# Performance work log

Hardware: AMD Instinct MI355X
Metric: run time of the kernel (lower is better)

Reference implementation:

```python
import jax, jax.numpy as jnp
import numpy as np

# GemNet sizes
N_EDGES = 80_000
N_TRIP = 640_000      # intermediate triplets (cbf rows)
N_QUAD = 1_280_000    # quadruplets
KMAX = 24             # max quadruplets per edge (padded)
NUM_SPH = 7
E_EDGE, E_QUAD, E_BIL, E_RBF, E_CBF, E_SBF = 128, 64, 64, 16, 16, 32

INV_SQRT_2 = 1.0 / np.sqrt(2.0)
SILU_SCALE = 1.0 / 0.6  # GemNet ScaledSiLU


def scaled_silu(x):
    return jax.nn.silu(x) * SILU_SCALE


def setup_inputs() -> dict:
    key = jax.random.key(0)
    ks = jax.random.split(key, 16)
    s = 0.05
    inp = {
        'm': jax.random.normal(ks[0], (N_EDGES, E_EDGE), jnp.float32),
        'rbf': jax.random.normal(ks[1], (N_EDGES, E_RBF), jnp.float32),
        'cbf': jax.random.normal(ks[2], (N_TRIP, E_CBF), jnp.float32),
        'sbf_W1': jax.random.normal(ks[3], (N_EDGES, E_SBF, NUM_SPH), jnp.float32) * s,
        'sbf_sph': jax.random.normal(ks[4], (N_EDGES, KMAX, NUM_SPH), jnp.float32) * s,
        # consistent ragged indexing: quadruplet q maps to edge q%N_EDGES at slot q//N_EDGES (< KMAX)
        'Kidx4': jnp.arange(N_QUAD, dtype=jnp.int32) // N_EDGES,
        'id4_reduce_ca': jnp.arange(N_QUAD, dtype=jnp.int32) % N_EDGES,
        'id_swap': jnp.arange(N_EDGES, dtype=jnp.int32).reshape(-1, 2)[:, ::-1].reshape(-1),
        'id4_expand_intm_db': jax.random.randint(ks[5], (N_TRIP,), 0, N_EDGES, jnp.int32),
        'id4_expand_abd': jax.random.randint(ks[6], (N_QUAD,), 0, N_TRIP, jnp.int32),
        # parameters (Dense layers are bias-free)
        'W_dense_db': jax.random.normal(ks[7], (E_EDGE, E_EDGE), jnp.float32) * s,
        'W_rbf': jax.random.normal(ks[8], (E_RBF, E_EDGE), jnp.float32) * s,
        'W_cbf': jax.random.normal(ks[9], (E_CBF, E_QUAD), jnp.float32) * s,
        'W_down': jax.random.normal(ks[10], (E_EDGE, E_QUAD), jnp.float32) * s,
        'W_bil': jax.random.normal(ks[11], (E_QUAD, E_SBF, E_BIL), jnp.float32) * s,
        'W_up_ca': jax.random.normal(ks[12], (E_BIL, E_EDGE), jnp.float32) * s,
        'W_up_ac': jax.random.normal(ks[13], (E_BIL, E_EDGE), jnp.float32) * s,
    }
    return inp


def reference(m, rbf, cbf, sbf_W1, sbf_sph,
              W_dense_db, W_rbf, W_cbf, W_down, W_bil, W_up_ca, W_up_ac,
              Kidx4, id_swap, id4_reduce_ca, id4_expand_intm_db, id4_expand_abd):
    # dense_db + Hadamard with projected rbf (ScalingFactor scale == 1.0 with scale_file=None)
    x_db = scaled_silu(m @ W_dense_db)           # (nEdges, E_EDGE)
    x_db = x_db * (rbf @ W_rbf)                  # scale_rbf (scale=1)
    x_db = scaled_silu(x_db @ W_down)            # (nEdges, E_QUAD)
    x_db = x_db[id4_expand_intm_db]              # (nTrip, E_QUAD)
    x_db = x_db * (cbf @ W_cbf)                  # scale_cbf (scale=1)
    x_db = x_db[id4_expand_abd]                  # (nQuad, E_QUAD)

    # EfficientInteractionBilinear: scatter quadruplets into (nEdges, Kmax, E_QUAD)
    n_edges, kmax = sbf_sph.shape[0], sbf_sph.shape[1]
    m2 = jnp.zeros((n_edges, kmax, x_db.shape[1]), x_db.dtype)
    m2 = m2.at[id4_reduce_ca, Kidx4].set(x_db)
    sum_k = jnp.einsum('eks,ekc->esc', sbf_sph, m2)    # (nEdges, NUM_SPH, E_QUAD)
    t = jnp.einsum('eis,esc->eic', sbf_W1, sum_k)      # (nEdges, E_SBF, E_QUAD)
    x = jnp.einsum('eic,cio->eo', t, W_bil)            # (nEdges, E_BIL); scale_sbf_sum (scale=1)

    x_ca = scaled_silu(x @ W_up_ca)              # (nEdges, E_EDGE)
    x_ac = scaled_silu(x @ W_up_ac)[id_swap]
    return (x_ca + x_ac) * INV_SQRT_2
```

## Files before the change

kernel.cpp:

```cpp
#include <hip/hip_runtime.h>
#include <hip/hip_bf16.h>

#define NEDGES 80000
#define NTRIP  640000
#define NQUAD  1280000

typedef __attribute__((ext_vector_type(8))) short short8;
typedef __attribute__((ext_vector_type(4))) float f32x4;
typedef __attribute__((ext_vector_type(2))) _Float16 half2v;
typedef __attribute__((ext_vector_type(8))) _Float16 half8v;

__device__ __forceinline__ unsigned short f2bf(float f) {
  __hip_bfloat16 h = __float2bfloat16(f);
  return reinterpret_cast<unsigned short&>(h);
}
__device__ __forceinline__ float bf2f(short s) {
  union { unsigned u; float f; } u;
  u.u = ((unsigned)(unsigned short)s) << 16;
  return u.f;
}
__device__ __forceinline__ float sSiLU(float x) {
  return x * (1.0f / 0.6f) / (1.0f + __expf(-x));
}

__device__ __forceinline__ void pack_one(const float* __restrict__ W,
                                         unsigned short* __restrict__ dst,
                                         int p, int NT, int Ksrc, int N) {
  int j = p & 7;
  int l = (p >> 3) & 63;
  int rest = p >> 9;
  int nt = rest % NT;
  int kb = rest / NT;
  int k = kb * 32 + ((l >> 4) << 3) + j;
  int n = nt * 16 + (l & 15);
  float v = (k < Ksrc) ? W[(size_t)k * N + n] : 0.0f;
  dst[p] = f2bf(v);
}

__global__ __launch_bounds__(256) void kpack(
    const float* __restrict__ Wd, const float* __restrict__ Wrbf,
    const float* __restrict__ Wdown, const float* __restrict__ Wbil,
    const float* __restrict__ Wupca, const float* __restrict__ Wupac,
    unsigned short* __restrict__ WdP, unsigned short* __restrict__ WrbfP,
    unsigned short* __restrict__ WdownP, unsigned short* __restrict__ WbilP,
    unsigned short* __restrict__ WupcaP, unsigned short* __restrict__ WupacP) {
  int idx = blockIdx.x * 256 + threadIdx.x;
  if (idx < 16384)        pack_one(Wd,    WdP,    idx,          8, 128,  128);
  else if (idx < 20480)   pack_one(Wrbf,  WrbfP,  idx - 16384,  8, 16,   128);
  else if (idx < 28672)   pack_one(Wdown, WdownP, idx - 20480,  4, 128,  64);
  else if (idx < 159744)  pack_one(Wbil,  WbilP,  idx - 28672,  4, 2048, 64);
  else if (idx < 167936)  pack_one(Wupca, WupcaP, idx - 159744, 8, 64,   128);
  else if (idx < 176128)  pack_one(Wupac, WupacP, idx - 167936, 8, 64,   128);
}

__global__ __launch_bounds__(256) void kA(
    const float* __restrict__ m, const float* __restrict__ rbf,
    const unsigned short* __restrict__ WdP, const unsigned short* __restrict__ WrbfP,
    const unsigned short* __restrict__ WdownP, unsigned short* __restrict__ x_down) {
  __shared__ unsigned short h_lds[4][16][136];
  const int tid = threadIdx.x;
  const int w = tid >> 6, l = tid & 63;
  const int el = l & 15, g = l >> 4;
  const int ebase = blockIdx.x * 64 + w * 16;

  short8 am[4];
  {
    const float* mrow = m + (size_t)(ebase + el) * 128 + g * 8;
#pragma unroll
    for (int kb = 0; kb < 4; ++kb) {
      const f32x4 lo = *reinterpret_cast<const f32x4*>(mrow + kb * 32);
      const f32x4 hi = *reinterpret_cast<const f32x4*>(mrow + kb * 32 + 4);
      short8 a;
      a[0] = f2bf(lo[0]); a[1] = f2bf(lo[1]); a[2] = f2bf(lo[2]); a[3] = f2bf(lo[3]);
      a[4] = f2bf(hi[0]); a[5] = f2bf(hi[1]); a[6] = f2bf(hi[2]); a[7] = f2bf(hi[3]);
      am[kb] = a;
    }
  }
  short8 ar;
  {
    const float* rrow = rbf + (size_t)(ebase + el) * 16 + (g & 1) * 8;
    const f32x4 lo = *reinterpret_cast<const f32x4*>(rrow);
    const f32x4 hi = *reinterpret_cast<const f32x4*>(rrow + 4);
    ar[0] = f2bf(lo[0]); ar[1] = f2bf(lo[1]); ar[2] = f2bf(lo[2]); ar[3] = f2bf(lo[3]);
    ar[4] = f2bf(hi[0]); ar[5] = f2bf(hi[1]); ar[6] = f2bf(hi[2]); ar[7] = f2bf(hi[3]);
  }

  f32x4 acc1[8], acc2[8];
  const f32x4 z = {0.f, 0.f, 0.f, 0.f};
#pragma unroll
  for (int nt = 0; nt < 8; ++nt) { acc1[nt] = z; acc2[nt] = z; }

#pragma unroll
  for (int kb = 0; kb < 4; ++kb) {
#pragma unroll
    for (int nt = 0; nt < 8; ++nt) {
      short8 b = *reinterpret_cast<const short8*>(WdP + (((kb * 8 + nt) * 64 + l) << 3));
      acc1[nt] = __builtin_amdgcn_mfma_f32_16x16x32_bf16(am[kb], b, acc1[nt], 0, 0, 0);
    }
  }
#pragma unroll
  for (int nt = 0; nt < 8; ++nt) {
    short8 b = *reinterpret_cast<const short8*>(WrbfP + ((nt * 64 + l) << 3));
    acc2[nt] = __builtin_amdgcn_mfma_f32_16x16x32_bf16(ar, b, acc2[nt], 0, 0, 0);
  }

#pragma unroll
  for (int nt = 0; nt < 8; ++nt)
#pragma unroll
    for (int r = 0; r < 4; ++r) {
      float h = sSiLU(acc1[nt][r]) * acc2[nt][r];
      h_lds[w][g * 4 + r][nt * 16 + el] = f2bf(h);
    }
  __syncthreads();

  f32x4 acc3[4];
#pragma unroll
  for (int nt = 0; nt < 4; ++nt) acc3[nt] = z;
#pragma unroll
  for (int kb = 0; kb < 4; ++kb) {
    short8 a = *reinterpret_cast<const short8*>(&h_lds[w][el][kb * 32 + g * 8]);
#pragma unroll
    for (int nt = 0; nt < 4; ++nt) {
      short8 b = *reinterpret_cast<const short8*>(WdownP + (((kb * 4 + nt) * 64 + l) << 3));
      acc3[nt] = __builtin_amdgcn_mfma_f32_16x16x32_bf16(a, b, acc3[nt], 0, 0, 0);
    }
  }
#pragma unroll
  for (int nt = 0; nt < 4; ++nt)
#pragma unroll
    for (int r = 0; r < 4; ++r)
      x_down[(size_t)(ebase + g * 4 + r) * 64 + nt * 16 + el] = f2bf(sSiLU(acc3[nt][r]));
}

__global__ __launch_bounds__(256) void kG(
    const float* __restrict__ cbf, const int* __restrict__ intm,
    const unsigned short* __restrict__ x_down, const float* __restrict__ Wcbf,
    unsigned short* __restrict__ y) {
  __shared__ float cbf_lds[4][16][16];
  const int tid = threadIdx.x;
  const int w = tid >> 6, c = tid & 63;
  const int wid = blockIdx.x * 4 + w;

  float wc[16];
#pragma unroll
  for (int r = 0; r < 16; ++r) wc[r] = Wcbf[r * 64 + c];

#pragma unroll
  for (int it = 0; it < 4; ++it) {
    const int t0 = (wid * 4 + it) * 16;

    const int ivv = intm[t0 + (c & 15)];
    const f32x4 cq = *reinterpret_cast<const f32x4*>(
        cbf + (size_t)(t0 + (c >> 2)) * 16 + (c & 3) * 4);
    *reinterpret_cast<f32x4*>(&cbf_lds[w][c >> 2][(c & 3) * 4]) = cq;

    int es[16];
#pragma unroll
    for (int k = 0; k < 16; ++k) es[k] = __builtin_amdgcn_readlane(ivv, k);

    unsigned short xr[16];
#pragma unroll
    for (int k = 0; k < 16; ++k) xr[k] = x_down[(size_t)es[k] * 64 + c];

#pragma unroll
    for (int j = 0; j < 16; ++j) {
      const f32x4* cr = reinterpret_cast<const f32x4*>(&cbf_lds[w][j][0]);
      const f32x4 q0 = cr[0], q1 = cr[1], q2 = cr[2], q3 = cr[3];
      float proj = 0.f;
#pragma unroll
      for (int r = 0; r < 4; ++r) {
        proj = fmaf(q0[r], wc[r], proj);
        proj = fmaf(q1[r], wc[4 + r], proj);
        proj = fmaf(q2[r], wc[8 + r], proj);
        proj = fmaf(q3[r], wc[12 + r], proj);
      }
      y[(size_t)(t0 + j) * 64 + c] = f2bf(bf2f((short)xr[j]) * proj);
    }
  }
}

__global__ __launch_bounds__(256) void kS2(
    const float* __restrict__ sph, const int* __restrict__ abd,
    const unsigned short* __restrict__ y, unsigned short* __restrict__ sumk) {
  __shared__ float sph_lds[4][172];
  const int tid = threadIdx.x;
  const int w = tid >> 6, c = tid & 63;
  const int wid = blockIdx.x * 4 + w;

#pragma unroll
  for (int it = 0; it < 8; ++it) {
    const int e = wid * 8 + it;

    const int tvv = abd[(size_t)(c & 15) * NEDGES + e];
    if (c < 42)
      *reinterpret_cast<f32x4*>(&sph_lds[w][c * 4]) =
          *reinterpret_cast<const f32x4*>(sph + (size_t)e * 168 + c * 4);

    int te[16];
#pragma unroll
    for (int k = 0; k < 16; ++k) te[k] = __builtin_amdgcn_readlane(tvv, k);

    unsigned short yv[16];
#pragma unroll
    for (int k = 0; k < 16; ++k) yv[k] = y[(size_t)te[k] * 64 + c];

    float sk[7] = {0.f, 0.f, 0.f, 0.f, 0.f, 0.f, 0.f};
#pragma unroll
    for (int k = 0; k < 16; ++k) {
      const float row = bf2f((short)yv[k]);
#pragma unroll
      for (int s = 0; s < 7; ++s) sk[s] = fmaf(sph_lds[w][k * 7 + s], row, sk[s]);
    }
    half8v sv;
#pragma unroll
    for (int s = 0; s < 7; ++s) sv[s] = (_Float16)sk[s];
    sv[7] = (_Float16)0.f;
    *reinterpret_cast<half8v*>(sumk + (size_t)e * 512 + c * 8) = sv;
  }
}

__global__ __launch_bounds__(256) void kS(
    const float* __restrict__ cbf, const float* __restrict__ sph,
    const int* __restrict__ abd, const int* __restrict__ intm,
    const unsigned short* __restrict__ x_down, const float* __restrict__ Wcbf,
    unsigned short* __restrict__ sumk) {
  __shared__ float cbf_lds[4][16][16];
  __shared__ int   te_lds[4][16];
  __shared__ float sph_lds[4][172];
  const int tid = threadIdx.x;
  const int w = tid >> 6, c = tid & 63;
  const int e = blockIdx.x * 4 + w;

  const int tvv = abd[(size_t)(c & 15) * NEDGES + e];
  if (c < 42)
    *reinterpret_cast<f32x4*>(&sph_lds[w][c * 4]) =
        *reinterpret_cast<const f32x4*>(sph + (size_t)e * 168 + c * 4);
  const int ivv = intm[tvv];
  if (c < 16) te_lds[w][c] = tvv;

  float wc[16];
#pragma unroll
  for (int r = 0; r < 16; ++r) wc[r] = Wcbf[r * 64 + c];

  int es[16];
#pragma unroll
  for (int k = 0; k < 16; ++k) es[k] = __builtin_amdgcn_readlane(ivv, k);

  const int tq = te_lds[w][c >> 2];
  const f32x4 cq = *reinterpret_cast<const f32x4*>(cbf + (size_t)tq * 16 + (c & 3) * 4);

  unsigned short xr[16];
#pragma unroll
  for (int k = 0; k < 16; ++k) xr[k] = x_down[(size_t)es[k] * 64 + c];

  *reinterpret_cast<f32x4*>(&cbf_lds[w][c >> 2][(c & 3) * 4]) = cq;

  float sk[7] = {0.f, 0.f, 0.f, 0.f, 0.f, 0.f, 0.f};
#pragma unroll
  for (int k = 0; k < 16; ++k) {
    const f32x4* cr = reinterpret_cast<const f32x4*>(&cbf_lds[w][k][0]);
    const f32x4 q0 = cr[0], q1 = cr[1], q2 = cr[2], q3 = cr[3];
    float proj = 0.f;
#pragma unroll
    for (int r = 0; r < 4; ++r) {
      proj = fmaf(q0[r], wc[r], proj);
      proj = fmaf(q1[r], wc[4 + r], proj);
      proj = fmaf(q2[r], wc[8 + r], proj);
      proj = fmaf(q3[r], wc[12 + r], proj);
    }
    const float row = bf2f((short)xr[k]) * proj;
#pragma unroll
    for (int s = 0; s < 7; ++s) sk[s] = fmaf(sph_lds[w][k * 7 + s], row, sk[s]);
  }
  short8 sv;
#pragma unroll
  for (int s = 0; s < 7; ++s) sv[s] = (short)f2bf(sk[s]);
  sv[7] = 0;
  *reinterpret_cast<short8*>(sumk + (size_t)e * 512 + c * 8) = sv;
}

__global__ __launch_bounds__(256, 4) void kB3(
    const float* __restrict__ sbfW1, const unsigned short* __restrict__ sumk,
    const unsigned short* __restrict__ WbilP, float* __restrict__ xpart) {
  __shared__ unsigned short stg[4][2][16][72];
  const int tid = threadIdx.x;
  const int w = tid >> 6, l = tid & 63;
  const int el = l & 15, g = l >> 4;
  const int gw = blockIdx.x * 4 + w;
  const int eb = gw >> 1, kh = gw & 1;
  const int ebase = eb * 16;
  const int sr = l >> 3, sq = l & 7;

  half2v w1h[32];
  {
    float w1f[56];
    const f32x4* wp = reinterpret_cast<const f32x4*>(sbfW1 + (size_t)(ebase + el) * 224 + g * 56);
#pragma unroll
    for (int qq = 0; qq < 14; ++qq) {
      f32x4 v = wp[qq];
      w1f[qq * 4 + 0] = v[0]; w1f[qq * 4 + 1] = v[1];
      w1f[qq * 4 + 2] = v[2]; w1f[qq * 4 + 3] = v[3];
    }
#pragma unroll
    for (int j = 0; j < 8; ++j) {
#pragma unroll
      for (int p = 0; p < 3; ++p) {
        half2v h;
        h[0] = (_Float16)w1f[j * 7 + 2 * p];
        h[1] = (_Float16)w1f[j * 7 + 2 * p + 1];
        w1h[j * 4 + p] = h;
      }
      half2v h;
      h[0] = (_Float16)w1f[j * 7 + 6];
      h[1] = (_Float16)0.f;
      w1h[j * 4 + 3] = h;
    }
  }

  const unsigned short* base = sumk + (size_t)ebase * 512 + kh * 256;
  short8 ld0 = *reinterpret_cast<const short8*>(base + (size_t)sr * 512 + sq * 8);
  short8 ld1 = *reinterpret_cast<const short8*>(base + (size_t)(sr + 8) * 512 + sq * 8);

  short8 bn0, bn1, bn2, bn3;
  {
    const unsigned short* bp = WbilP + (((kh * 32 * 4) * 64 + l) << 3);
    bn0 = *reinterpret_cast<const short8*>(bp);
    bn1 = *reinterpret_cast<const short8*>(bp + (64 << 3));
    bn2 = *reinterpret_cast<const short8*>(bp + (128 << 3));
    bn3 = *reinterpret_cast<const short8*>(bp + (192 << 3));
  }

  const f32x4 z = {0.f, 0.f, 0.f, 0.f};
  f32x4 acc[4];
#pragma unroll
  for (int nt = 0; nt < 4; ++nt) acc[nt] = z;

#pragma unroll
  for (int s = 0; s < 4; ++s) {
    const int b = s & 1;
    *reinterpret_cast<short8*>(&stg[w][b][sr][sq * 8]) = ld0;
    *reinterpret_cast<short8*>(&stg[w][b][sr + 8][sq * 8]) = ld1;
    if (s < 3) {
      ld0 = *reinterpret_cast<const short8*>(base + (size_t)sr * 512 + (s + 1) * 64 + sq * 8);
      ld1 = *reinterpret_cast<const short8*>(base + (size_t)(sr + 8) * 512 + (s + 1) * 64 + sq * 8);
    }
#pragma unroll
    for (int kk = 0; kk < 8; ++kk) {
      const short8 bc0 = bn0, bc1 = bn1, bc2 = bn2, bc3 = bn3;
      if (!(s == 3 && kk == 7)) {
        const int kbn = kh * 32 + s * 8 + kk + 1;
        const unsigned short* bp = WbilP + (((kbn * 4) * 64 + l) << 3);
        bn0 = *reinterpret_cast<const short8*>(bp);
        bn1 = *reinterpret_cast<const short8*>(bp + (64 << 3));
        bn2 = *reinterpret_cast<const short8*>(bp + (128 << 3));
        bn3 = *reinterpret_cast<const short8*>(bp + (192 << 3));
      }

      const half8v skv = *reinterpret_cast<const half8v*>(&stg[w][b][el][kk * 8]);
      half2v sp0, sp1, sp2, sp3;
      sp0[0] = skv[0]; sp0[1] = skv[1];
      sp1[0] = skv[2]; sp1[1] = skv[3];
      sp2[0] = skv[4]; sp2[1] = skv[5];
      sp3[0] = skv[6]; sp3[1] = skv[7];

      short8 a;
#pragma unroll
      for (int j = 0; j < 8; ++j) {
        float t = 0.f;
        t = __builtin_amdgcn_fdot2(w1h[j * 4 + 0], sp0, t, false);
        t = __builtin_amdgcn_fdot2(w1h[j * 4 + 1], sp1, t, false);
        t = __builtin_amdgcn_fdot2(w1h[j * 4 + 2], sp2, t, false);
        t = __builtin_amdgcn_fdot2(w1h[j * 4 + 3], sp3, t, false);
        a[j] = (short)f2bf(t);
      }
      acc[0] = __builtin_amdgcn_mfma_f32_16x16x32_bf16(a, bc0, acc[0], 0, 0, 0);
      acc[1] = __builtin_amdgcn_mfma_f32_16x16x32_bf16(a, bc1, acc[1], 0, 0, 0);
      acc[2] = __builtin_amdgcn_mfma_f32_16x16x32_bf16(a, bc2, acc[2], 0, 0, 0);
      acc[3] = __builtin_amdgcn_mfma_f32_16x16x32_bf16(a, bc3, acc[3], 0, 0, 0);
    }
  }

  float* po = xpart + (size_t)kh * (NEDGES * 64);
#pragma unroll
  for (int nt = 0; nt < 4; ++nt)
#pragma unroll
    for (int r = 0; r < 4; ++r)
      po[(size_t)(ebase + g * 4 + r) * 64 + nt * 16 + el] = acc[nt][r];
}

__global__ __launch_bounds__(256) void kU(
    const float* __restrict__ xpart, const unsigned short* __restrict__ WupcaP,
    const unsigned short* __restrict__ WupacP, float* __restrict__ out) {
  const int tid = threadIdx.x;
  const int w = tid >> 6, l = tid & 63;
  const int el = l & 15, g = l >> 4;
  const int ebase = (blockIdx.x * 4 + w) * 16;

  const float* p0 = xpart + (size_t)(ebase + el) * 64;
  const float* p1 = p0 + (size_t)NEDGES * 64;

  const f32x4 z = {0.f, 0.f, 0.f, 0.f};
  f32x4 aca[8], acb[8];
#pragma unroll
  for (int nt = 0; nt < 8; ++nt) { aca[nt] = z; acb[nt] = z; }

#pragma unroll
  for (int kb = 0; kb < 2; ++kb) {
    const f32x4 a0 = *reinterpret_cast<const f32x4*>(p0 + kb * 32 + g * 8);
    const f32x4 a1 = *reinterpret_cast<const f32x4*>(p0 + kb * 32 + g * 8 + 4);
    const f32x4 b0 = *reinterpret_cast<const f32x4*>(p1 + kb * 32 + g * 8);
    const f32x4 b1 = *reinterpret_cast<const f32x4*>(p1 + kb * 32 + g * 8 + 4);
    short8 a;
#pragma unroll
    for (int j = 0; j < 4; ++j) {
      a[j]     = (short)f2bf(a0[j] + b0[j]);
      a[4 + j] = (short)f2bf(a1[j] + b1[j]);
    }
#pragma unroll
    for (int nt = 0; nt < 8; ++nt) {
      short8 w1 = *reinterpret_cast<const short8*>(WupcaP + (((kb * 8 + nt) * 64 + l) << 3));
      short8 w2 = *reinterpret_cast<const short8*>(WupacP + (((kb * 8 + nt) * 64 + l) << 3));
      aca[nt] = __builtin_amdgcn_mfma_f32_16x16x32_bf16(a, w1, aca[nt], 0, 0, 0);
      acb[nt] = __builtin_amdgcn_mfma_f32_16x16x32_bf16(a, w2, acb[nt], 0, 0, 0);
    }
  }
  const float inv = 0.70710678118654752f;
#pragma unroll
  for (int nt = 0; nt < 8; ++nt)
#pragma unroll
    for (int r = 0; r < 4; ++r) {
      float v = (sSiLU(aca[nt][r]) + sSiLU(acb[nt][r ^ 1])) * inv;
      out[(size_t)(ebase + g * 4 + r) * 128 + nt * 16 + el] = v;
    }
}

__global__ __launch_bounds__(256) void kB2f(
    const float* __restrict__ sbfW1, const unsigned short* __restrict__ sumk,
    const unsigned short* __restrict__ WbilP, const unsigned short* __restrict__ WupcaP,
    const unsigned short* __restrict__ WupacP, float* __restrict__ out) {
  __shared__ unsigned short sk_lds[4][16][520];
  __shared__ unsigned short x_lds[4][16][72];
  const int tid = threadIdx.x;
  const int w = tid >> 6, l = tid & 63;
  const int el = l & 15, g = l >> 4;
  const int ebase = blockIdx.x * 64 + w * 16;

#pragma unroll
  for (int i = 0; i < 16; ++i) {
    const short8 v = *reinterpret_cast<const short8*>(sumk + (size_t)(ebase + i) * 512 + l * 8);
    *reinterpret_cast<short8*>(&sk_lds[w][i][l * 8]) = v;
  }

  float w1r[56];
  {
    const f32x4* wp = reinterpret_cast<const f32x4*>(sbfW1 + (size_t)(ebase + el) * 224 + g * 56);
#pragma unroll
    for (int qq = 0; qq < 14; ++qq) {
      f32x4 v = wp[qq];
      w1r[qq * 4 + 0] = v[0]; w1r[qq * 4 + 1] = v[1];
      w1r[qq * 4 + 2] = v[2]; w1r[qq * 4 + 3] = v[3];
    }
  }
  __syncthreads();

  const f32x4 z = {0.f, 0.f, 0.f, 0.f};
  f32x4 acc[4];
#pragma unroll
  for (int nt = 0; nt < 4; ++nt) acc[nt] = z;

#pragma unroll 4
  for (int kb = 0; kb < 64; ++kb) {
    const short8 skv = *reinterpret_cast<const short8*>(&sk_lds[w][el][kb * 8]);
    float skf[7];
#pragma unroll
    for (int s = 0; s < 7; ++s) skf[s] = bf2f(skv[s]);
    short8 a;
#pragma unroll
    for (int j = 0; j < 8; ++j) {
      float t = 0.f;
#pragma unroll
      for (int s = 0; s < 7; ++s) t = fmaf(w1r[j * 7 + s], skf[s], t);
      a[j] = (short)f2bf(t);
    }
    const unsigned short* bp = WbilP + (((kb * 4) * 64 + l) << 3);
#pragma unroll
    for (int nt = 0; nt < 4; ++nt) {
      short8 b = *reinterpret_cast<const short8*>(bp + ((nt * 64) << 3));
      acc[nt] = __builtin_amdgcn_mfma_f32_16x16x32_bf16(a, b, acc[nt], 0, 0, 0);
    }
  }

#pragma unroll
  for (int nt = 0; nt < 4; ++nt)
#pragma unroll
    for (int r = 0; r < 4; ++r)
      x_lds[w][g * 4 + r][nt * 16 + el] = f2bf(acc[nt][r]);
  __syncthreads();

  f32x4 aca[8], acb[8];
#pragma unroll
  for (int nt = 0; nt < 8; ++nt) { aca[nt] = z; acb[nt] = z; }
#pragma unroll
  for (int kb = 0; kb < 2; ++kb) {
    short8 a = *reinterpret_cast<const short8*>(&x_lds[w][el][kb * 32 + g * 8]);
#pragma unroll
    for (int nt = 0; nt < 8; ++nt) {
      short8 b1 = *reinterpret_cast<const short8*>(WupcaP + (((kb * 8 + nt) * 64 + l) << 3));
      short8 b2 = *reinterpret_cast<const short8*>(WupacP + (((kb * 8 + nt) * 64 + l) << 3));
      aca[nt] = __builtin_amdgcn_mfma_f32_16x16x32_bf16(a, b1, aca[nt], 0, 0, 0);
      acb[nt] = __builtin_amdgcn_mfma_f32_16x16x32_bf16(a, b2, acb[nt], 0, 0, 0);
    }
  }
  const float inv = 0.70710678118654752f;
#pragma unroll
  for (int nt = 0; nt < 8; ++nt)
#pragma unroll
    for (int r = 0; r < 4; ++r) {
      float v = (sSiLU(aca[nt][r]) + sSiLU(acb[nt][r ^ 1])) * inv;
      out[(size_t)(ebase + g * 4 + r) * 128 + nt * 16 + el] = v;
    }
}

extern "C" void kernel_launch(void* const* d_in, const int* in_sizes, int n_in,
                              void* d_out, int out_size, void* d_ws, size_t ws_size,
                              hipStream_t stream) {
  const float* m     = (const float*)d_in[0];
  const float* rbf   = (const float*)d_in[1];
  const float* cbf   = (const float*)d_in[2];
  const float* sbfW1 = (const float*)d_in[3];
  const float* sph   = (const float*)d_in[4];
  const int* intm = (const int*)d_in[8];
  const int* abd  = (const int*)d_in[9];
  const float* Wd    = (const float*)d_in[10];
  const float* Wrbf  = (const float*)d_in[11];
  const float* Wcbf  = (const float*)d_in[12];
  const float* Wdown = (const float*)d_in[13];
  const float* Wbil  = (const float*)d_in[14];
  const float* Wupca = (const float*)d_in[15];
  const float* Wupac = (const float*)d_in[16];

  char* ws = (char*)d_ws;
  unsigned short* WdP    = (unsigned short*)(ws + 0);
  unsigned short* WrbfP  = (unsigned short*)(ws + 32768);
  unsigned short* WdownP = (unsigned short*)(ws + 40960);
  unsigned short* WbilP  = (unsigned short*)(ws + 57344);
  unsigned short* WupcaP = (unsigned short*)(ws + 319488);
  unsigned short* WupacP = (unsigned short*)(ws + 335872);
  unsigned short* x_down = (unsigned short*)(ws + 352256);
  unsigned short* y      = (unsigned short*)(ws + 352256 + 10240000);
  unsigned short* sumk   = (unsigned short*)(ws + 352256 + 10240000 + 81920000);
  float*          xpart  = (float*)y;
  unsigned short* sumk_f = y;
  const size_t needed_split = 352256ull + 10240000ull + 81920000ull + 81920000ull;

  kpack<<<688, 256, 0, stream>>>(Wd, Wrbf, Wdown, Wbil, Wupca, Wupac,
                                 WdP, WrbfP, WdownP, WbilP, WupcaP, WupacP);
  kA<<<1250, 256, 0, stream>>>(m, rbf, WdP, WrbfP, WdownP, x_down);
  if (ws_size >= needed_split) {
    kG<<<2500, 256, 0, stream>>>(cbf, intm, x_down, Wcbf, y);
    kS2<<<2500, 256, 0, stream>>>(sph, abd, y, sumk);
    kB3<<<2500, 256, 0, stream>>>(sbfW1, sumk, WbilP, xpart);
    kU<<<1250, 256, 0, stream>>>(xpart, WupcaP, WupacP, (float*)d_out);
  } else {
    kS<<<20000, 256, 0, stream>>>(cbf, sph, abd, intm, x_down, Wcbf, sumk_f);
    kB2f<<<1250, 256, 0, stream>>>(sbfW1, sumk_f, WbilP, WupcaP, WupacP, (float*)d_out);
  }
}
```

Measured before the change: 239.7 us.

## Fuse bilinear and up-projection kernels, reducing k-halves through shared memory

Merges the bilinear contraction kernel with the up-projection/SiLU kernel. The two k-half partial results for each 16-edge tile are now summed through LDS within the block instead of being written to and re-read from a global fp32 buffer. This removes a large global round trip and one launch. In exchange it adds LDS usage and a block barrier, and it rounds the partials to bf16 before summing them.

```diff
diff --git a/kernel.cpp b/kernel.cpp
--- a/kernel.cpp
+++ b/kernel.cpp
@@ -279,10 +279,12 @@
   *reinterpret_cast<short8*>(sumk + (size_t)e * 512 + c * 8) = sv;
 }
 
-__global__ __launch_bounds__(256, 4) void kB3(
+__global__ __launch_bounds__(256, 4) void kBU(
     const float* __restrict__ sbfW1, const unsigned short* __restrict__ sumk,
-    const unsigned short* __restrict__ WbilP, float* __restrict__ xpart) {
+    const unsigned short* __restrict__ WbilP, const unsigned short* __restrict__ WupcaP,
+    const unsigned short* __restrict__ WupacP, float* __restrict__ out) {
   __shared__ unsigned short stg[4][2][16][72];
+  __shared__ unsigned short xl[4][16][72];
   const int tid = threadIdx.x;
   const int w = tid >> 6, l = tid & 63;
   const int el = l & 15, g = l >> 4;
@@ -380,57 +382,43 @@
     }
   }
 
-  float* po = xpart + (size_t)kh * (NEDGES * 64);
 #pragma unroll
   for (int nt = 0; nt < 4; ++nt)
 #pragma unroll
     for (int r = 0; r < 4; ++r)
-      po[(size_t)(ebase + g * 4 + r) * 64 + nt * 16 + el] = acc[nt][r];
-}
-
-__global__ __launch_bounds__(256) void kU(
-    const float* __restrict__ xpart, const unsigned short* __restrict__ WupcaP,
-    const unsigned short* __restrict__ WupacP, float* __restrict__ out) {
-  const int tid = threadIdx.x;
-  const int w = tid >> 6, l = tid & 63;
-  const int el = l & 15, g = l >> 4;
-  const int ebase = (blockIdx.x * 4 + w) * 16;
-
-  const float* p0 = xpart + (size_t)(ebase + el) * 64;
-  const float* p1 = p0 + (size_t)NEDGES * 64;
-
-  const f32x4 z = {0.f, 0.f, 0.f, 0.f};
-  f32x4 aca[8], acb[8];
-#pragma unroll
-  for (int nt = 0; nt < 8; ++nt) { aca[nt] = z; acb[nt] = z; }
+      xl[w][g * 4 + r][nt * 16 + el] = f2bf(acc[nt][r]);
+  __syncthreads();
+
+  const int wa = w & ~1, wb = wa + 1;
+  f32x4 aca[4], acb[4];
+#pragma unroll
+  for (int nt = 0; nt < 4; ++nt) { aca[nt] = z; acb[nt] = z; }
 
 #pragma unroll
   for (int kb = 0; kb < 2; ++kb) {
-    const f32x4 a0 = *reinterpret_cast<const f32x4*>(p0 + kb * 32 + g * 8);
-    const f32x4 a1 = *reinterpret_cast<const f32x4*>(p0 + kb * 32 + g * 8 + 4);
-    const f32x4 b0 = *reinterpret_cast<const f32x4*>(p1 + kb * 32 + g * 8);
-    const f32x4 b1 = *reinterpret_cast<const f32x4*>(p1 + kb * 32 + g * 8 + 4);
+    const short8 p0 = *reinterpret_cast<const short8*>(&xl[wa][el][kb * 32 + g * 8]);
+    const short8 p1 = *reinterpret_cast<const short8*>(&xl[wb][el][kb * 32 + g * 8]);
     short8 a;
 #pragma unroll
-    for (int j = 0; j < 4; ++j) {
-      a[j]     = (short)f2bf(a0[j] + b0[j]);
-      a[4 + j] = (short)f2bf(a1[j] + b1[j]);
-    }
-#pragma unroll
-    for (int nt = 0; nt < 8; ++nt) {
-      short8 w1 = *reinterpret_cast<const short8*>(WupcaP + (((kb * 8 + nt) * 64 + l) << 3));
-      short8 w2 = *reinterpret_cast<const short8*>(WupacP + (((kb * 8 + nt) * 64 + l) << 3));
-      aca[nt] = __builtin_amdgcn_mfma_f32_16x16x32_bf16(a, w1, aca[nt], 0, 0, 0);
-      acb[nt] = __builtin_amdgcn_mfma_f32_16x16x32_bf16(a, w2, acb[nt], 0, 0, 0);
+    for (int j = 0; j < 8; ++j)
+      a[j] = (short)f2bf(bf2f(p0[j]) + bf2f(p1[j]));
+#pragma unroll
+    for (int nt = 0; nt < 4; ++nt) {
+      const int ntg = kh * 4 + nt;
+      short8 b1 = *reinterpret_cast<const short8*>(WupcaP + (((kb * 8 + ntg) * 64 + l) << 3));
+      short8 b2 = *reinterpret_cast<const short8*>(WupacP + (((kb * 8 + ntg) * 64 + l) << 3));
+      aca[nt] = __builtin_amdgcn_mfma_f32_16x16x32_bf16(a, b1, aca[nt], 0, 0, 0);
+      acb[nt] = __builtin_amdgcn_mfma_f32_16x16x32_bf16(a, b2, acb[nt], 0, 0, 0);
     }
   }
   const float inv = 0.70710678118654752f;
 #pragma unroll
-  for (int nt = 0; nt < 8; ++nt)
+  for (int nt = 0; nt < 4; ++nt)
 #pragma unroll
     for (int r = 0; r < 4; ++r) {
+      const int ntg = kh * 4 + nt;
       float v = (sSiLU(aca[nt][r]) + sSiLU(acb[nt][r ^ 1])) * inv;
-      out[(size_t)(ebase + g * 4 + r) * 128 + nt * 16 + el] = v;
+      out[(size_t)(ebase + g * 4 + r) * 128 + ntg * 16 + el] = v;
     }
 }
 
@@ -549,7 +537,6 @@
   unsigned short* x_down = (unsigned short*)(ws + 352256);
   unsigned short* y      = (unsigned short*)(ws + 352256 + 10240000);
   unsigned short* sumk   = (unsigned short*)(ws + 352256 + 10240000 + 81920000);
-  float*          xpart  = (float*)y;
   unsigned short* sumk_f = y;
   const size_t needed_split = 352256ull + 10240000ull + 81920000ull + 81920000ull;
 
@@ -559,8 +546,7 @@
   if (ws_size >= needed_split) {
     kG<<<2500, 256, 0, stream>>>(cbf, intm, x_down, Wcbf, y);
     kS2<<<2500, 256, 0, stream>>>(sph, abd, y, sumk);
-    kB3<<<2500, 256, 0, stream>>>(sbfW1, sumk, WbilP, xpart);
-    kU<<<1250, 256, 0, stream>>>(xpart, WupcaP, WupacP, (float*)d_out);
+    kBU<<<2500, 256, 0, stream>>>(sbfW1, sumk, WbilP, WupcaP, WupacP, (float*)d_out);
   } else {
     kS<<<20000, 256, 0, stream>>>(cbf, sph, abd, intm, x_down, Wcbf, sumk_f);
     kB2f<<<1250, 256, 0, stream>>>(sbfW1, sumk_f, WbilP, WupcaP, WupacP, (float*)d_out);
```

Result: faster. 231.7 us (-3.3%).
